# Optimization experiments

Hardware: AMD Instinct MI355X
Metric: run time of the kernel (lower is better)

Reference implementation:

```python
import jax, jax.numpy as jnp
import numpy as np

N = 50000        # nodes
E = 800000       # edges
IN_DIM, HID, OUT = 512, 256, 128
EPS = 1e-5       # PyG LayerNorm eps (added to std)


def setup_inputs() -> dict:
    key = jax.random.key(0)
    ks = jax.random.split(key, 24)
    def lin(k, i, o, scale=0.05):
        kw, kb = jax.random.split(k)
        return (jax.random.normal(kw, (i, o), jnp.float32) * scale,
                jax.random.normal(kb, (o,), jnp.float32) * scale)
    x = jax.random.normal(ks[0], (N, IN_DIM), jnp.float32)
    edge_index = jax.random.randint(ks[1], (2, E), 0, N, jnp.int64)
    Wq1, bq1 = lin(ks[2], IN_DIM, HID)
    Wk1, bk1 = lin(ks[3], IN_DIM, HID)
    Wv1, bv1 = lin(ks[4], IN_DIM, HID)
    Ws1, bs1 = lin(ks[5], IN_DIM, HID)
    g1 = jnp.ones((HID,), jnp.float32)
    be1 = jnp.zeros((HID,), jnp.float32)
    Wq2, bq2 = lin(ks[6], HID, OUT)
    Wk2, bk2 = lin(ks[7], HID, OUT)
    Wv2, bv2 = lin(ks[8], HID, OUT)
    Ws2, bs2 = lin(ks[9], HID, OUT)
    g2 = jnp.ones((OUT,), jnp.float32)
    be2 = jnp.zeros((OUT,), jnp.float32)
    return dict(x=x, Wq1=Wq1, bq1=bq1, Wk1=Wk1, bk1=bk1, Wv1=Wv1, bv1=bv1,
                Ws1=Ws1, bs1=bs1, g1=g1, be1=be1,
                Wq2=Wq2, bq2=bq2, Wk2=Wk2, bk2=bk2, Wv2=Wv2, bv2=bv2,
                Ws2=Ws2, bs2=bs2, g2=g2, be2=be2, edge_index=edge_index)


def transformer_conv(x, edge_index, Wq, bq, Wk, bk, Wv, bv, Ws, bs):
    # PyG TransformerConv, heads=1, concat=True, root_weight=True
    src, dst = edge_index[0], edge_index[1]
    n = x.shape[0]
    d = Wq.shape[1]
    q = x @ Wq + bq                               # [N, d]
    k = x @ Wk + bk
    v = x @ Wv + bv
    score = (q[dst] * k[src]).sum(-1) / jnp.sqrt(jnp.asarray(d, x.dtype))  # [E]
    m = jax.ops.segment_max(score, dst, num_segments=n)     # per-target max
    e = jnp.exp(score - m[dst])
    denom = jax.ops.segment_sum(e, dst, num_segments=n)
    alpha = e / denom[dst]                         # scatter-softmax over in-edges
    agg = jax.ops.segment_sum(alpha[:, None] * v[src], dst, num_segments=n)
    return agg + (x @ Ws + bs)                     # root/skip connection


def graph_layer_norm(h, w, b):
    # PyG LayerNorm mode='graph', no batch: normalize over ALL entries
    h = h - h.mean()
    return h / (h.std() + EPS) * w + b


def reference(x, Wq1, bq1, Wk1, bk1, Wv1, bv1, Ws1, bs1, g1, be1,
              Wq2, bq2, Wk2, bk2, Wv2, bv2, Ws2, bs2, g2, be2, edge_index):
    a1 = graph_layer_norm(
        transformer_conv(x, edge_index, Wq1, bq1, Wk1, bk1, Wv1, bv1, Ws1, bs1),
        g1, be1)
    h1 = jax.nn.elu(a1)  # ELU(alpha=1.0)
    h2 = graph_layer_norm(
        transformer_conv(h1, edge_index, Wq2, bq2, Wk2, bk2, Wv2, bv2, Ws2, bs2),
        g2, be2)
    return h2
```

## Files before the change

kernel.cpp:

```cpp
#include <hip/hip_runtime.h>
#include <stdint.h>
#include <math.h>

#define IN_DIM 512
#define HID    256
#define OUTD   128
#define LN_EPS 1e-5f

typedef unsigned short u16;
typedef unsigned int   u32;
typedef short short8 __attribute__((ext_vector_type(8)));
typedef float f32x4  __attribute__((ext_vector_type(4)));

__device__ __forceinline__ float bf2f(u32 h) {
  union { u32 u; float f; } c; c.u = h << 16; return c.f;
}
__device__ __forceinline__ u16 f2bf(float f) {
  union { float f; u32 u; } c; c.f = f;
  u32 u = c.u;
  return (u16)((u + 0x7FFFu + ((u >> 16) & 1u)) >> 16);
}

__device__ __forceinline__ void gload_lds16(const void* g, void* l) {
  __builtin_amdgcn_global_load_lds((const __attribute__((address_space(1))) void*)g,
                                   (__attribute__((address_space(3))) void*)l, 16, 0, 0);
}

__global__ void k_cvt_f32_bf16_v4(const float* __restrict__ in, u16* __restrict__ out, int n4) {
  int i = blockIdx.x * blockDim.x + threadIdx.x;
  if (i >= n4) return;
  const float4 v = ((const float4*)in)[i];
  ushort4 o;
  o.x = f2bf(v.x); o.y = f2bf(v.y); o.z = f2bf(v.z); o.w = f2bf(v.w);
  ((ushort4*)out)[i] = o;
}

__global__ void k_transpose_w(const float* __restrict__ in, u16* __restrict__ out, int K, int Nw) {
  int idx = blockIdx.x * blockDim.x + threadIdx.x;
  if (idx >= K * Nw) return;
  int n = idx / K, k = idx - n * K;
  out[idx] = f2bf(in[(size_t)k * Nw + n]);
}

__global__ void k_concat4(const float* __restrict__ b0, const float* __restrict__ b1,
                          const float* __restrict__ b2, const float* __restrict__ b3,
                          float* __restrict__ out, int H) {
  int i = blockIdx.x * blockDim.x + threadIdx.x;
  if (i >= 4 * H) return;
  const float* s = (i < H) ? b0 : (i < 2 * H) ? b1 : (i < 3 * H) ? b2 : b3;
  out[i] = s[i & (H - 1)];
}

__global__ void k_hist(const int* __restrict__ dst, int* __restrict__ deg, int E) {
  int e = blockIdx.x * blockDim.x + threadIdx.x;
  if (e < E) atomicAdd(&deg[dst[e]], 1);
}

__global__ void k_block_sum(const int* __restrict__ deg, int* __restrict__ bsum, int n) {
  __shared__ int sm[256];
  int i = blockIdx.x * 256 + threadIdx.x;
  sm[threadIdx.x] = (i < n) ? deg[i] : 0;
  __syncthreads();
  for (int off = 128; off > 0; off >>= 1) {
    if (threadIdx.x < off) sm[threadIdx.x] += sm[threadIdx.x + off];
    __syncthreads();
  }
  if (threadIdx.x == 0) bsum[blockIdx.x] = sm[0];
}

__global__ void k_scan_bsum(const int* __restrict__ bsum, int* __restrict__ boff, int nb) {
  __shared__ int sm[256];
  int t = threadIdx.x;
  int v = (t < nb) ? bsum[t] : 0;
  sm[t] = v;
  __syncthreads();
  for (int off = 1; off < 256; off <<= 1) {
    int tmp = (t >= off) ? sm[t - off] : 0;
    __syncthreads();
    sm[t] += tmp;
    __syncthreads();
  }
  if (t < nb) boff[t] = sm[t] - v;
}

__global__ void k_scan_final(const int* __restrict__ deg, const int* __restrict__ boff,
                             int* __restrict__ offsets, int n, int total) {
  __shared__ int sm[256];
  int t = threadIdx.x;
  int i = blockIdx.x * 256 + t;
  int v = (i < n) ? deg[i] : 0;
  sm[t] = v;
  __syncthreads();
  for (int off = 1; off < 256; off <<= 1) {
    int tmp = (t >= off) ? sm[t - off] : 0;
    __syncthreads();
    sm[t] += tmp;
    __syncthreads();
  }
  if (i < n) offsets[i] = boff[blockIdx.x] + sm[t] - v;
  if (i == 0) offsets[n] = total;
}

__global__ void k_copy_int(const int* __restrict__ in, int* __restrict__ out, int n) {
  int i = blockIdx.x * blockDim.x + threadIdx.x;
  if (i < n) out[i] = in[i];
}

__global__ void k_scatter(const int* __restrict__ src, const int* __restrict__ dst,
                          int* __restrict__ cursor, int* __restrict__ ssrc, int E) {
  int e = blockIdx.x * blockDim.x + threadIdx.x;
  if (e >= E) return;
  int d = dst[e];
  int pos = atomicAdd(&cursor[d], 1);
  ssrc[pos] = src[e];
}

__global__ __launch_bounds__(256) void k_gemm_bf16_nt(
    const u16* __restrict__ A, const u16* __restrict__ Bt, const float* __restrict__ bias,
    u16* __restrict__ C, int M, int K, int Nt) {
  __shared__ __align__(16) u16 As[128 * 32];
  __shared__ __align__(16) u16 Bs[128 * 32];
  const int tid = threadIdx.x;
  const int bm0 = blockIdx.x * 128;
  const int bn0 = blockIdx.y * 128;
  const int wave = tid >> 6, lane = tid & 63;
  const int q = lane >> 4, r16 = lane & 15;
  const int wm = (wave >> 1) * 64, wn = (wave & 1) * 64;

  f32x4 acc[4][4];
#pragma unroll
  for (int i = 0; i < 4; i++)
#pragma unroll
    for (int j = 0; j < 4; j++) acc[i][j] = (f32x4){0.f, 0.f, 0.f, 0.f};

  const int r0 = tid >> 2;
  const int c0 = (tid & 3) * 8;

  for (int kt = 0; kt < K; kt += 32) {
#pragma unroll
    for (int h = 0; h < 2; ++h) {
      int row = r0 + h * 64;
      gload_lds16(A + (size_t)(bm0 + row) * K + kt + c0, &As[row * 32 + c0]);
      gload_lds16(Bt + (size_t)(bn0 + row) * K + kt + c0, &Bs[row * 32 + c0]);
    }
    __syncthreads();
    short8 af[4], bfr[4];
#pragma unroll
    for (int i = 0; i < 4; i++) af[i] = *(const short8*)(&As[(wm + i * 16 + r16) * 32 + q * 8]);
#pragma unroll
    for (int j = 0; j < 4; j++) bfr[j] = *(const short8*)(&Bs[(wn + j * 16 + r16) * 32 + q * 8]);
#pragma unroll
    for (int i = 0; i < 4; i++)
#pragma unroll
      for (int j = 0; j < 4; j++)
        acc[i][j] = __builtin_amdgcn_mfma_f32_16x16x32_bf16(af[i], bfr[j], acc[i][j], 0, 0, 0);
    __syncthreads();
  }

#pragma unroll
  for (int i = 0; i < 4; i++) {
#pragma unroll
    for (int r = 0; r < 4; r++) {
      int grow = bm0 + wm + i * 16 + q * 4 + r;
      if (grow >= M) continue;
      size_t rbase = (size_t)grow * Nt;
#pragma unroll
      for (int j = 0; j < 4; j++) {
        int gcol = bn0 + wn + j * 16 + r16;
        float v = acc[i][j][r] + bias[gcol];
        C[rbase + gcol] = f2bf(v);
      }
    }
  }
}

template <int VPL>
__device__ __forceinline__ void load_bf(const u16* __restrict__ p, int lane, float* f) {
  if constexpr (VPL == 4) {
    uint2 r = *(const uint2*)(p + lane * 4);
    f[0] = bf2f(r.x & 0xffffu); f[1] = bf2f(r.x >> 16);
    f[2] = bf2f(r.y & 0xffffu); f[3] = bf2f(r.y >> 16);
  } else {
    u32 r = *(const u32*)(p + lane * 2);
    f[0] = bf2f(r & 0xffffu); f[1] = bf2f(r >> 16);
  }
}

template <int H, bool OUT_BF16>
__global__ __launch_bounds__(256) void k_conv(
    const u16* __restrict__ qkvs, const int* __restrict__ offsets,
    const int* __restrict__ ssrc, u16* __restrict__ out_bf,
    float* __restrict__ out_f, int n, float scale) {
  constexpr int VPL = H / 64;
  int gw = (blockIdx.x * blockDim.x + threadIdx.x) >> 6;
  int lane = threadIdx.x & 63;
  if (gw >= n) return;
  const u16* base = qkvs + (size_t)gw * (4 * H);
  float qf[VPL];
  load_bf<VPL>(base, lane, qf);
  int beg = offsets[gw], end = offsets[gw + 1];
  float m = -INFINITY, l = 0.f;
  float agg[VPL];
#pragma unroll
  for (int w = 0; w < VPL; w++) agg[w] = 0.f;

  int i = beg;
  for (; i + 4 <= end; i += 4) {
    int s0 = ssrc[i], s1 = ssrc[i + 1], s2 = ssrc[i + 2], s3 = ssrc[i + 3];
    const u16* k0p = qkvs + (size_t)s0 * (4 * H) + H;
    const u16* k1p = qkvs + (size_t)s1 * (4 * H) + H;
    const u16* k2p = qkvs + (size_t)s2 * (4 * H) + H;
    const u16* k3p = qkvs + (size_t)s3 * (4 * H) + H;
    float k0[VPL], k1[VPL], k2[VPL], k3[VPL];
    float v0[VPL], v1[VPL], v2[VPL], v3[VPL];
    load_bf<VPL>(k0p, lane, k0);
    load_bf<VPL>(k1p, lane, k1);
    load_bf<VPL>(k2p, lane, k2);
    load_bf<VPL>(k3p, lane, k3);
    load_bf<VPL>(k0p + H, lane, v0);
    load_bf<VPL>(k1p + H, lane, v1);
    load_bf<VPL>(k2p + H, lane, v2);
    load_bf<VPL>(k3p + H, lane, v3);
    float d0 = 0.f, d1 = 0.f, d2 = 0.f, d3 = 0.f;
#pragma unroll
    for (int w = 0; w < VPL; w++) {
      d0 += qf[w] * k0[w]; d1 += qf[w] * k1[w];
      d2 += qf[w] * k2[w]; d3 += qf[w] * k3[w];
    }
#pragma unroll
    for (int off = 32; off > 0; off >>= 1) {
      d0 += __shfl_xor(d0, off, 64);
      d1 += __shfl_xor(d1, off, 64);
      d2 += __shfl_xor(d2, off, 64);
      d3 += __shfl_xor(d3, off, 64);
    }
    d0 *= scale; d1 *= scale; d2 *= scale; d3 *= scale;
    float cm = fmaxf(fmaxf(d0, d1), fmaxf(d2, d3));
    float nm = fmaxf(m, cm);
    float sc = __expf(m - nm);
    float p0 = __expf(d0 - nm), p1 = __expf(d1 - nm);
    float p2 = __expf(d2 - nm), p3 = __expf(d3 - nm);
    m = nm;
    l = l * sc + (p0 + p1) + (p2 + p3);
#pragma unroll
    for (int w = 0; w < VPL; w++)
      agg[w] = agg[w] * sc + p0 * v0[w] + p1 * v1[w] + p2 * v2[w] + p3 * v3[w];
  }
  for (; i < end; ++i) {
    int s = ssrc[i];
    const u16* kb = qkvs + (size_t)s * (4 * H) + H;
    float kf[VPL], vf[VPL];
    load_bf<VPL>(kb, lane, kf);
    load_bf<VPL>(kb + H, lane, vf);
    float d = 0.f;
#pragma unroll
    for (int w = 0; w < VPL; w++) d += qf[w] * kf[w];
#pragma unroll
    for (int off = 32; off > 0; off >>= 1) d += __shfl_xor(d, off, 64);
    float score = d * scale;
    float nm = fmaxf(m, score);
    float sc = __expf(m - nm);
    float p = __expf(score - nm);
    m = nm;
    l = l * sc + p;
#pragma unroll
    for (int w = 0; w < VPL; w++) agg[w] = agg[w] * sc + p * vf[w];
  }

  float sf[VPL];
  load_bf<VPL>(base + 3 * H, lane, sf);
  float inv = (end > beg) ? 1.f / l : 0.f;
#pragma unroll
  for (int w = 0; w < VPL; w++) {
    float r = agg[w] * inv + sf[w];
    if (OUT_BF16) out_bf[(size_t)gw * H + lane * VPL + w] = f2bf(r);
    else out_f[(size_t)gw * H + lane * VPL + w] = r;
  }
}

__global__ void k_stats_bf16(const u16* __restrict__ a, int n, double* __restrict__ st) {
  float s = 0.f, s2 = 0.f;
  for (int i = blockIdx.x * blockDim.x + threadIdx.x; i < n; i += gridDim.x * blockDim.x) {
    float v = bf2f(a[i]);
    s += v; s2 += v * v;
  }
  __shared__ float sm[256], sm2[256];
  sm[threadIdx.x] = s; sm2[threadIdx.x] = s2;
  __syncthreads();
  for (int off = 128; off > 0; off >>= 1) {
    if (threadIdx.x < off) { sm[threadIdx.x] += sm[threadIdx.x + off]; sm2[threadIdx.x] += sm2[threadIdx.x + off]; }
    __syncthreads();
  }
  if (threadIdx.x == 0) { atomicAdd(&st[0], (double)sm[0]); atomicAdd(&st[1], (double)sm2[0]); }
}

__global__ void k_stats_f32(const float* __restrict__ a, int n, double* __restrict__ st) {
  float s = 0.f, s2 = 0.f;
  for (int i = blockIdx.x * blockDim.x + threadIdx.x; i < n; i += gridDim.x * blockDim.x) {
    float v = a[i];
    s += v; s2 += v * v;
  }
  __shared__ float sm[256], sm2[256];
  sm[threadIdx.x] = s; sm2[threadIdx.x] = s2;
  __syncthreads();
  for (int off = 128; off > 0; off >>= 1) {
    if (threadIdx.x < off) { sm[threadIdx.x] += sm[threadIdx.x + off]; sm2[threadIdx.x] += sm2[threadIdx.x + off]; }
    __syncthreads();
  }
  if (threadIdx.x == 0) { atomicAdd(&st[0], (double)sm[0]); atomicAdd(&st[1], (double)sm2[0]); }
}

__global__ void k_finstats(const double* __restrict__ st, float* __restrict__ fs, double cnt) {
  double mu = st[0] / cnt;
  double var = st[1] / cnt - mu * mu;
  if (var < 0.0) var = 0.0;
  fs[0] = (float)mu;
  fs[1] = (float)(1.0 / (sqrt(var) + (double)LN_EPS));
}

__global__ void k_norm_elu_bf16(const u16* __restrict__ a, const float* __restrict__ g,
                                const float* __restrict__ b, const float* __restrict__ fs,
                                u16* __restrict__ out, int n, int Hmask) {
  int i = blockIdx.x * blockDim.x + threadIdx.x;
  if (i >= n) return;
  int c = i & Hmask;
  float y = (bf2f(a[i]) - fs[0]) * fs[1] * g[c] + b[c];
  y = (y > 0.f) ? y : (__expf(y) - 1.f);
  out[i] = f2bf(y);
}

__global__ void k_norm_f32(float* __restrict__ a, const float* __restrict__ g,
                           const float* __restrict__ b, const float* __restrict__ fs,
                           int n, int Hmask) {
  int i = blockIdx.x * blockDim.x + threadIdx.x;
  if (i >= n) return;
  int c = i & Hmask;
  a[i] = (a[i] - fs[0]) * fs[1] * g[c] + b[c];
}

extern "C" void kernel_launch(void* const* d_in, const int* in_sizes, int n_in,
                              void* d_out, int out_size, void* d_ws, size_t ws_size,
                              hipStream_t stream) {
  const float* x   = (const float*)d_in[0];
  const float* Wq1 = (const float*)d_in[1];  const float* bq1 = (const float*)d_in[2];
  const float* Wk1 = (const float*)d_in[3];  const float* bk1 = (const float*)d_in[4];
  const float* Wv1 = (const float*)d_in[5];  const float* bv1 = (const float*)d_in[6];
  const float* Ws1 = (const float*)d_in[7];  const float* bs1 = (const float*)d_in[8];
  const float* g1  = (const float*)d_in[9];  const float* be1 = (const float*)d_in[10];
  const float* Wq2 = (const float*)d_in[11]; const float* bq2 = (const float*)d_in[12];
  const float* Wk2 = (const float*)d_in[13]; const float* bk2 = (const float*)d_in[14];
  const float* Wv2 = (const float*)d_in[15]; const float* bv2 = (const float*)d_in[16];
  const float* Ws2 = (const float*)d_in[17]; const float* bs2 = (const float*)d_in[18];
  const float* g2  = (const float*)d_in[19]; const float* be2 = (const float*)d_in[20];
  const int*   ei  = (const int*)d_in[21];

  const int N = in_sizes[0] / IN_DIM;
  const int E = in_sizes[21] / 2;
  const int* esrc = ei;
  const int* edst = ei + E;

  char* w = (char*)d_ws;
  auto carve = [&](size_t bytes) { char* p = w; w += (bytes + 255) & ~(size_t)255; return p; };
  u16* x_bf  = (u16*)carve((size_t)N * IN_DIM * 2);
  u16* Wt1   = (u16*)carve((size_t)4 * HID * IN_DIM * 2);
  u16* Wt2   = (u16*)carve((size_t)4 * OUTD * HID * 2);
  float* bc1 = (float*)carve(4 * HID * 4);
  float* bc2 = (float*)carve(4 * OUTD * 4);
  u16* qkvs1 = (u16*)carve((size_t)N * 4 * HID * 2);
  u16* a1    = (u16*)carve((size_t)N * HID * 2);
  int* deg   = (int*)carve((size_t)(N + 1) * 4);
  int* offs  = (int*)carve((size_t)(N + 1) * 4);
  int* cur   = (int*)carve((size_t)(N + 1) * 4);
  int* ssrc  = (int*)carve((size_t)E * 4);
  int* bsum  = (int*)carve(1024);
  int* boff  = (int*)carve(1024);
  double* st = (double*)carve(64);
  float* fs  = (float*)carve(64);
  u16* h1    = x_bf;
  u16* qkvs2 = qkvs1;

  hipMemsetAsync(deg, 0, (size_t)N * 4, stream);
  hipMemsetAsync(st, 0, 64, stream);

  int n4 = N * IN_DIM / 4;
  k_cvt_f32_bf16_v4<<<(n4 + 255) / 256, 256, 0, stream>>>(x, x_bf, n4);
  k_transpose_w<<<(IN_DIM * HID + 255) / 256, 256, 0, stream>>>(Wq1, Wt1 + 0 * (size_t)HID * IN_DIM, IN_DIM, HID);
  k_transpose_w<<<(IN_DIM * HID + 255) / 256, 256, 0, stream>>>(Wk1, Wt1 + 1 * (size_t)HID * IN_DIM, IN_DIM, HID);
  k_transpose_w<<<(IN_DIM * HID + 255) / 256, 256, 0, stream>>>(Wv1, Wt1 + 2 * (size_t)HID * IN_DIM, IN_DIM, HID);
  k_transpose_w<<<(IN_DIM * HID + 255) / 256, 256, 0, stream>>>(Ws1, Wt1 + 3 * (size_t)HID * IN_DIM, IN_DIM, HID);
  k_concat4<<<(4 * HID + 255) / 256, 256, 0, stream>>>(bq1, bk1, bv1, bs1, bc1, HID);
  k_transpose_w<<<(HID * OUTD + 255) / 256, 256, 0, stream>>>(Wq2, Wt2 + 0 * (size_t)OUTD * HID, HID, OUTD);
  k_transpose_w<<<(HID * OUTD + 255) / 256, 256, 0, stream>>>(Wk2, Wt2 + 1 * (size_t)OUTD * HID, HID, OUTD);
  k_transpose_w<<<(HID * OUTD + 255) / 256, 256, 0, stream>>>(Wv2, Wt2 + 2 * (size_t)OUTD * HID, HID, OUTD);
  k_transpose_w<<<(HID * OUTD + 255) / 256, 256, 0, stream>>>(Ws2, Wt2 + 3 * (size_t)OUTD * HID, HID, OUTD);
  k_concat4<<<(4 * OUTD + 255) / 256, 256, 0, stream>>>(bq2, bk2, bv2, bs2, bc2, OUTD);

  int nb = (N + 255) / 256;
  k_hist<<<(E + 255) / 256, 256, 0, stream>>>(edst, deg, E);
  k_block_sum<<<nb, 256, 0, stream>>>(deg, bsum, N);
  k_scan_bsum<<<1, 256, 0, stream>>>(bsum, boff, nb);
  k_scan_final<<<nb, 256, 0, stream>>>(deg, boff, offs, N, E);
  k_copy_int<<<nb, 256, 0, stream>>>(offs, cur, N);
  k_scatter<<<(E + 255) / 256, 256, 0, stream>>>(esrc, edst, cur, ssrc, E);

  dim3 gg1((N + 127) / 128, (4 * HID) / 128);
  k_gemm_bf16_nt<<<gg1, 256, 0, stream>>>(x_bf, Wt1, bc1, qkvs1, N, IN_DIM, 4 * HID);
  k_conv<HID, true><<<(N + 3) / 4, 256, 0, stream>>>(qkvs1, offs, ssrc, a1, nullptr, N,
                                                     1.0f / sqrtf((float)HID));
  k_stats_bf16<<<2048, 256, 0, stream>>>(a1, N * HID, st);
  k_finstats<<<1, 1, 0, stream>>>(st, fs, (double)N * HID);
  k_norm_elu_bf16<<<(N * HID + 255) / 256, 256, 0, stream>>>(a1, g1, be1, fs, h1, N * HID, HID - 1);

  dim3 gg2((N + 127) / 128, (4 * OUTD) / 128);
  k_gemm_bf16_nt<<<gg2, 256, 0, stream>>>(h1, Wt2, bc2, qkvs2, N, HID, 4 * OUTD);
  k_conv<OUTD, false><<<(N + 3) / 4, 256, 0, stream>>>(qkvs2, offs, ssrc, nullptr, (float*)d_out, N,
                                                       1.0f / sqrtf((float)OUTD));
  k_stats_f32<<<2048, 256, 0, stream>>>((const float*)d_out, N * OUTD, st + 2);
  k_finstats<<<1, 1, 0, stream>>>(st + 2, fs + 2, (double)N * OUTD);
  k_norm_f32<<<(N * OUTD + 255) / 256, 256, 0, stream>>>((float*)d_out, g2, be2, fs + 2, N * OUTD, OUTD - 1);
}
```

Before: 772.2 us.

## Fuse prep kernels, split edges across sub-waves in conv, fold stats into conv

Merges the input conversion, weight transposes and bias concatenation into one prep kernel, and the cursor copy into the scan. Restructures the attention conv so each wave handles several edges at once, with sub-groups of lanes loading 16-byte K/V slices, followed by a cross-subgroup online-softmax merge. The layer-norm sum and sum-of-squares are now accumulated inside the conv, which removes the separate stats pass. The normalize kernels are vectorized. The aim is fewer launches, fewer memory passes and better gather memory-level parallelism, at the cost of extra shuffle merges and more complex tail handling.

```diff
diff --git a/kernel.cpp b/kernel.cpp
--- a/kernel.cpp
+++ b/kernel.cpp
@@ -26,29 +26,54 @@
                                    (__attribute__((address_space(3))) void*)l, 16, 0, 0);
 }
 
-__global__ void k_cvt_f32_bf16_v4(const float* __restrict__ in, u16* __restrict__ out, int n4) {
-  int i = blockIdx.x * blockDim.x + threadIdx.x;
-  if (i >= n4) return;
-  const float4 v = ((const float4*)in)[i];
-  ushort4 o;
-  o.x = f2bf(v.x); o.y = f2bf(v.y); o.z = f2bf(v.z); o.w = f2bf(v.w);
-  ((ushort4*)out)[i] = o;
-}
-
-__global__ void k_transpose_w(const float* __restrict__ in, u16* __restrict__ out, int K, int Nw) {
-  int idx = blockIdx.x * blockDim.x + threadIdx.x;
-  if (idx >= K * Nw) return;
-  int n = idx / K, k = idx - n * K;
-  out[idx] = f2bf(in[(size_t)k * Nw + n]);
-}
-
-__global__ void k_concat4(const float* __restrict__ b0, const float* __restrict__ b1,
-                          const float* __restrict__ b2, const float* __restrict__ b3,
-                          float* __restrict__ out, int H) {
-  int i = blockIdx.x * blockDim.x + threadIdx.x;
-  if (i >= 4 * H) return;
-  const float* s = (i < H) ? b0 : (i < 2 * H) ? b1 : (i < 3 * H) ? b2 : b3;
-  out[i] = s[i & (H - 1)];
+__global__ void k_prep(const float* __restrict__ x, u16* __restrict__ x_bf, int n4,
+                       const float* __restrict__ Wq1, const float* __restrict__ Wk1,
+                       const float* __restrict__ Wv1, const float* __restrict__ Ws1,
+                       const float* __restrict__ Wq2, const float* __restrict__ Wk2,
+                       const float* __restrict__ Wv2, const float* __restrict__ Ws2,
+                       u16* __restrict__ Wt1, u16* __restrict__ Wt2,
+                       const float* __restrict__ bq1, const float* __restrict__ bk1,
+                       const float* __restrict__ bv1, const float* __restrict__ bs1,
+                       const float* __restrict__ bq2, const float* __restrict__ bk2,
+                       const float* __restrict__ bv2, const float* __restrict__ bs2,
+                       float* __restrict__ bc1, float* __restrict__ bc2) {
+  const int W1SZ = 4 * HID * IN_DIM;
+  const int W2SZ = 4 * OUTD * HID;
+  int id = blockIdx.x * blockDim.x + threadIdx.x;
+  if (id < n4) {
+    const float4 v = ((const float4*)x)[id];
+    ushort4 o;
+    o.x = f2bf(v.x); o.y = f2bf(v.y); o.z = f2bf(v.z); o.w = f2bf(v.w);
+    ((ushort4*)x_bf)[id] = o;
+    return;
+  }
+  id -= n4;
+  if (id < W1SZ) {
+    int mat = id >> 17, r = id & 131071;
+    int n = r >> 9, k = r & 511;
+    const float* src = (mat == 0) ? Wq1 : (mat == 1) ? Wk1 : (mat == 2) ? Wv1 : Ws1;
+    Wt1[id] = f2bf(src[k * HID + n]);
+    return;
+  }
+  id -= W1SZ;
+  if (id < W2SZ) {
+    int mat = id >> 15, r = id & 32767;
+    int n = r >> 8, k = r & 255;
+    const float* src = (mat == 0) ? Wq2 : (mat == 1) ? Wk2 : (mat == 2) ? Wv2 : Ws2;
+    Wt2[id] = f2bf(src[k * OUTD + n]);
+    return;
+  }
+  id -= W2SZ;
+  if (id < 4 * HID) {
+    const float* s = (id < HID) ? bq1 : (id < 2 * HID) ? bk1 : (id < 3 * HID) ? bv1 : bs1;
+    bc1[id] = s[id & (HID - 1)];
+    return;
+  }
+  id -= 4 * HID;
+  if (id < 4 * OUTD) {
+    const float* s = (id < OUTD) ? bq2 : (id < 2 * OUTD) ? bk2 : (id < 3 * OUTD) ? bv2 : bs2;
+    bc2[id] = s[id & (OUTD - 1)];
+  }
 }
 
 __global__ void k_hist(const int* __restrict__ dst, int* __restrict__ deg, int E) {
@@ -84,7 +109,8 @@
 }
 
 __global__ void k_scan_final(const int* __restrict__ deg, const int* __restrict__ boff,
-                             int* __restrict__ offsets, int n, int total) {
+                             int* __restrict__ offsets, int* __restrict__ cur,
+                             int n, int total) {
   __shared__ int sm[256];
   int t = threadIdx.x;
   int i = blockIdx.x * 256 + t;
@@ -97,13 +123,12 @@
     sm[t] += tmp;
     __syncthreads();
   }
-  if (i < n) offsets[i] = boff[blockIdx.x] + sm[t] - v;
+  if (i < n) {
+    int o = boff[blockIdx.x] + sm[t] - v;
+    offsets[i] = o;
+    cur[i] = o;
+  }
   if (i == 0) offsets[n] = total;
-}
-
-__global__ void k_copy_int(const int* __restrict__ in, int* __restrict__ out, int n) {
-  int i = blockIdx.x * blockDim.x + threadIdx.x;
-  if (i < n) out[i] = in[i];
 }
 
 __global__ void k_scatter(const int* __restrict__ src, const int* __restrict__ dst,
@@ -174,140 +199,193 @@
   }
 }
 
-template <int VPL>
-__device__ __forceinline__ void load_bf(const u16* __restrict__ p, int lane, float* f) {
-  if constexpr (VPL == 4) {
-    uint2 r = *(const uint2*)(p + lane * 4);
-    f[0] = bf2f(r.x & 0xffffu); f[1] = bf2f(r.x >> 16);
-    f[2] = bf2f(r.y & 0xffffu); f[3] = bf2f(r.y >> 16);
-  } else {
-    u32 r = *(const u32*)(p + lane * 2);
-    f[0] = bf2f(r & 0xffffu); f[1] = bf2f(r >> 16);
-  }
-}
-
 template <int H, bool OUT_BF16>
 __global__ __launch_bounds__(256) void k_conv(
     const u16* __restrict__ qkvs, const int* __restrict__ offsets,
     const int* __restrict__ ssrc, u16* __restrict__ out_bf,
-    float* __restrict__ out_f, int n, float scale) {
-  constexpr int VPL = H / 64;
-  int gw = (blockIdx.x * blockDim.x + threadIdx.x) >> 6;
-  int lane = threadIdx.x & 63;
-  if (gw >= n) return;
-  const u16* base = qkvs + (size_t)gw * (4 * H);
-  float qf[VPL];
-  load_bf<VPL>(base, lane, qf);
-  int beg = offsets[gw], end = offsets[gw + 1];
+    float* __restrict__ out_f, int n, float scale, double* __restrict__ st) {
+  constexpr int SUBW = H / 8;
+  constexpr int EPW = 64 / SUBW;
+  constexpr int U = (H == 256) ? 4 : 2;
+
+  const int wave = threadIdx.x >> 6;
+  const int lane = threadIdx.x & 63;
+  const int sub = lane & (SUBW - 1);
+  const int subid = lane >> ((H == 256) ? 5 : 4);
+  const int gw = blockIdx.x * 4 + wave;
+
   float m = -INFINITY, l = 0.f;
-  float agg[VPL];
-#pragma unroll
-  for (int w = 0; w < VPL; w++) agg[w] = 0.f;
-
-  int i = beg;
-  for (; i + 4 <= end; i += 4) {
-    int s0 = ssrc[i], s1 = ssrc[i + 1], s2 = ssrc[i + 2], s3 = ssrc[i + 3];
-    const u16* k0p = qkvs + (size_t)s0 * (4 * H) + H;
-    const u16* k1p = qkvs + (size_t)s1 * (4 * H) + H;
-    const u16* k2p = qkvs + (size_t)s2 * (4 * H) + H;
-    const u16* k3p = qkvs + (size_t)s3 * (4 * H) + H;
-    float k0[VPL], k1[VPL], k2[VPL], k3[VPL];
-    float v0[VPL], v1[VPL], v2[VPL], v3[VPL];
-    load_bf<VPL>(k0p, lane, k0);
-    load_bf<VPL>(k1p, lane, k1);
-    load_bf<VPL>(k2p, lane, k2);
-    load_bf<VPL>(k3p, lane, k3);
-    load_bf<VPL>(k0p + H, lane, v0);
-    load_bf<VPL>(k1p + H, lane, v1);
-    load_bf<VPL>(k2p + H, lane, v2);
-    load_bf<VPL>(k3p + H, lane, v3);
-    float d0 = 0.f, d1 = 0.f, d2 = 0.f, d3 = 0.f;
-#pragma unroll
-    for (int w = 0; w < VPL; w++) {
-      d0 += qf[w] * k0[w]; d1 += qf[w] * k1[w];
-      d2 += qf[w] * k2[w]; d3 += qf[w] * k3[w];
-    }
-#pragma unroll
-    for (int off = 32; off > 0; off >>= 1) {
-      d0 += __shfl_xor(d0, off, 64);
-      d1 += __shfl_xor(d1, off, 64);
-      d2 += __shfl_xor(d2, off, 64);
-      d3 += __shfl_xor(d3, off, 64);
-    }
-    d0 *= scale; d1 *= scale; d2 *= scale; d3 *= scale;
-    float cm = fmaxf(fmaxf(d0, d1), fmaxf(d2, d3));
-    float nm = fmaxf(m, cm);
-    float sc = __expf(m - nm);
-    float p0 = __expf(d0 - nm), p1 = __expf(d1 - nm);
-    float p2 = __expf(d2 - nm), p3 = __expf(d3 - nm);
-    m = nm;
-    l = l * sc + (p0 + p1) + (p2 + p3);
-#pragma unroll
-    for (int w = 0; w < VPL; w++)
-      agg[w] = agg[w] * sc + p0 * v0[w] + p1 * v1[w] + p2 * v2[w] + p3 * v3[w];
-  }
-  for (; i < end; ++i) {
-    int s = ssrc[i];
-    const u16* kb = qkvs + (size_t)s * (4 * H) + H;
-    float kf[VPL], vf[VPL];
-    load_bf<VPL>(kb, lane, kf);
-    load_bf<VPL>(kb + H, lane, vf);
-    float d = 0.f;
-#pragma unroll
-    for (int w = 0; w < VPL; w++) d += qf[w] * kf[w];
-#pragma unroll
-    for (int off = 32; off > 0; off >>= 1) d += __shfl_xor(d, off, 64);
-    float score = d * scale;
-    float nm = fmaxf(m, score);
-    float sc = __expf(m - nm);
-    float p = __expf(score - nm);
-    m = nm;
-    l = l * sc + p;
-#pragma unroll
-    for (int w = 0; w < VPL; w++) agg[w] = agg[w] * sc + p * vf[w];
-  }
-
-  float sf[VPL];
-  load_bf<VPL>(base + 3 * H, lane, sf);
-  float inv = (end > beg) ? 1.f / l : 0.f;
-#pragma unroll
-  for (int w = 0; w < VPL; w++) {
-    float r = agg[w] * inv + sf[w];
-    if (OUT_BF16) out_bf[(size_t)gw * H + lane * VPL + w] = f2bf(r);
-    else out_f[(size_t)gw * H + lane * VPL + w] = r;
-  }
-}
-
-__global__ void k_stats_bf16(const u16* __restrict__ a, int n, double* __restrict__ st) {
+  float agg[8];
+#pragma unroll
+  for (int w = 0; w < 8; w++) agg[w] = 0.f;
+  float r[8];
+#pragma unroll
+  for (int w = 0; w < 8; w++) r[w] = 0.f;
+  bool live = gw < n;
+  int beg = 0, end = 0;
+
+  if (live) {
+    const u16* base = qkvs + (size_t)gw * (4 * H);
+    float qf[8];
+    {
+      uint4 qv = *(const uint4*)(base + sub * 8);
+      const u32 qa[4] = {qv.x, qv.y, qv.z, qv.w};
+#pragma unroll
+      for (int w = 0; w < 4; w++) {
+        qf[2 * w] = bf2f(qa[w] & 0xffffu);
+        qf[2 * w + 1] = bf2f(qa[w] >> 16);
+      }
+    }
+    beg = offsets[gw]; end = offsets[gw + 1];
+
+    int i = beg;
+    for (; i + EPW * U <= end; i += EPW * U) {
+      uint4 kq[U], vq[U];
+      const u16* kp[U];
+#pragma unroll
+      for (int u = 0; u < U; u++) {
+        int s = ssrc[i + u * EPW + subid];
+        kp[u] = qkvs + (size_t)s * (4 * H) + H;
+      }
+#pragma unroll
+      for (int u = 0; u < U; u++) kq[u] = *(const uint4*)(kp[u] + sub * 8);
+#pragma unroll
+      for (int u = 0; u < U; u++) vq[u] = *(const uint4*)(kp[u] + H + sub * 8);
+      float d[U];
+#pragma unroll
+      for (int u = 0; u < U; u++) {
+        const u32 ka[4] = {kq[u].x, kq[u].y, kq[u].z, kq[u].w};
+        float dd = 0.f;
+#pragma unroll
+        for (int w = 0; w < 4; w++) {
+          dd += qf[2 * w] * bf2f(ka[w] & 0xffffu);
+          dd += qf[2 * w + 1] * bf2f(ka[w] >> 16);
+        }
+        d[u] = dd;
+      }
+#pragma unroll
+      for (int off = SUBW / 2; off > 0; off >>= 1)
+#pragma unroll
+        for (int u = 0; u < U; u++) d[u] += __shfl_xor(d[u], off, 64);
+      float cm = -INFINITY;
+#pragma unroll
+      for (int u = 0; u < U; u++) { d[u] *= scale; cm = fmaxf(cm, d[u]); }
+      float nm = fmaxf(m, cm);
+      float sc = __expf(m - nm);
+      float p[U];
+      float ps = 0.f;
+#pragma unroll
+      for (int u = 0; u < U; u++) { p[u] = __expf(d[u] - nm); ps += p[u]; }
+      m = nm;
+      l = l * sc + ps;
+#pragma unroll
+      for (int w = 0; w < 8; w++) {
+        float a = agg[w] * sc;
+#pragma unroll
+        for (int u = 0; u < U; u++) {
+          const u32 vv = ((const u32*)&vq[u])[w >> 1];
+          float vf = bf2f((w & 1) ? (vv >> 16) : (vv & 0xffffu));
+          a += p[u] * vf;
+        }
+        agg[w] = a;
+      }
+    }
+    for (; i < end; i += EPW) {
+      int e = i + subid;
+      bool act = e < end;
+      int s = act ? ssrc[e] : ssrc[i];
+      const u16* kp = qkvs + (size_t)s * (4 * H) + H;
+      uint4 kq = *(const uint4*)(kp + sub * 8);
+      uint4 vq = *(const uint4*)(kp + H + sub * 8);
+      const u32 ka[4] = {kq.x, kq.y, kq.z, kq.w};
+      float d = 0.f;
+#pragma unroll
+      for (int w = 0; w < 4; w++) {
+        d += qf[2 * w] * bf2f(ka[w] & 0xffffu);
+        d += qf[2 * w + 1] * bf2f(ka[w] >> 16);
+      }
+#pragma unroll
+      for (int off = SUBW / 2; off > 0; off >>= 1) d += __shfl_xor(d, off, 64);
+      d = act ? d * scale : -INFINITY;
+      float nm = fmaxf(m, d);
+      bool dead = (nm == -INFINITY);
+      float sc = dead ? 1.f : __expf(m - nm);
+      float p = dead ? 0.f : __expf(d - nm);
+      m = nm;
+      l = l * sc + p;
+#pragma unroll
+      for (int w = 0; w < 8; w++) {
+        const u32 vv = ((const u32*)&vq)[w >> 1];
+        float vf = bf2f((w & 1) ? (vv >> 16) : (vv & 0xffffu));
+        agg[w] = agg[w] * sc + p * vf;
+      }
+    }
+
+#pragma unroll
+    for (int off = SUBW; off < 64; off <<= 1) {
+      float mo = __shfl_xor(m, off, 64);
+      float lo = __shfl_xor(l, off, 64);
+      float M = fmaxf(m, mo);
+      float sa = (M == -INFINITY) ? 0.f : __expf(m - M);
+      float sb = (M == -INFINITY) ? 0.f : __expf(mo - M);
+      l = l * sa + lo * sb;
+#pragma unroll
+      for (int w = 0; w < 8; w++) {
+        float ao = __shfl_xor(agg[w], off, 64);
+        agg[w] = agg[w] * sa + ao * sb;
+      }
+      m = M;
+    }
+
+    float sf[8];
+    {
+      uint4 sv = *(const uint4*)(base + 3 * H + sub * 8);
+      const u32 sa[4] = {sv.x, sv.y, sv.z, sv.w};
+#pragma unroll
+      for (int w = 0; w < 4; w++) {
+        sf[2 * w] = bf2f(sa[w] & 0xffffu);
+        sf[2 * w + 1] = bf2f(sa[w] >> 16);
+      }
+    }
+    float inv = (end > beg) ? 1.f / l : 0.f;
+#pragma unroll
+    for (int w = 0; w < 8; w++) r[w] = agg[w] * inv + sf[w];
+    if (subid == 0) {
+      if (OUT_BF16) {
+        uint4 o;
+        u32* op = (u32*)&o;
+#pragma unroll
+        for (int w = 0; w < 4; w++)
+          op[w] = (u32)f2bf(r[2 * w]) | ((u32)f2bf(r[2 * w + 1]) << 16);
+        *(uint4*)(out_bf + (size_t)gw * H + sub * 8) = o;
+      } else {
+        float4 o0 = {r[0], r[1], r[2], r[3]};
+        float4 o1 = {r[4], r[5], r[6], r[7]};
+        *(float4*)(out_f + (size_t)gw * H + sub * 8) = o0;
+        *(float4*)(out_f + (size_t)gw * H + sub * 8 + 4) = o1;
+      }
+    }
+  }
+
   float s = 0.f, s2 = 0.f;
-  for (int i = blockIdx.x * blockDim.x + threadIdx.x; i < n; i += gridDim.x * blockDim.x) {
-    float v = bf2f(a[i]);
-    s += v; s2 += v * v;
-  }
-  __shared__ float sm[256], sm2[256];
-  sm[threadIdx.x] = s; sm2[threadIdx.x] = s2;
+  if (live && subid == 0) {
+#pragma unroll
+    for (int w = 0; w < 8; w++) { s += r[w]; s2 += r[w] * r[w]; }
+  }
+#pragma unroll
+  for (int off = 32; off > 0; off >>= 1) {
+    s += __shfl_xor(s, off, 64);
+    s2 += __shfl_xor(s2, off, 64);
+  }
+  __shared__ float bs_[8];
+  if (lane == 0) { bs_[wave * 2] = s; bs_[wave * 2 + 1] = s2; }
   __syncthreads();
-  for (int off = 128; off > 0; off >>= 1) {
-    if (threadIdx.x < off) { sm[threadIdx.x] += sm[threadIdx.x + off]; sm2[threadIdx.x] += sm2[threadIdx.x + off]; }
-    __syncthreads();
-  }
-  if (threadIdx.x == 0) { atomicAdd(&st[0], (double)sm[0]); atomicAdd(&st[1], (double)sm2[0]); }
-}
-
-__global__ void k_stats_f32(const float* __restrict__ a, int n, double* __restrict__ st) {
-  float s = 0.f, s2 = 0.f;
-  for (int i = blockIdx.x * blockDim.x + threadIdx.x; i < n; i += gridDim.x * blockDim.x) {
-    float v = a[i];
-    s += v; s2 += v * v;
-  }
-  __shared__ float sm[256], sm2[256];
-  sm[threadIdx.x] = s; sm2[threadIdx.x] = s2;
-  __syncthreads();
-  for (int off = 128; off > 0; off >>= 1) {
-    if (threadIdx.x < off) { sm[threadIdx.x] += sm[threadIdx.x + off]; sm2[threadIdx.x] += sm2[threadIdx.x + off]; }
-    __syncthreads();
-  }
-  if (threadIdx.x == 0) { atomicAdd(&st[0], (double)sm[0]); atomicAdd(&st[1], (double)sm2[0]); }
+  if (wave == 0 && lane == 0) {
+    float ts = bs_[0] + bs_[2] + bs_[4] + bs_[6];
+    float ts2 = bs_[1] + bs_[3] + bs_[5] + bs_[7];
+    atomicAdd(&st[0], (double)ts);
+    atomicAdd(&st[1], (double)ts2);
+  }
 }
 
 __global__ void k_finstats(const double* __restrict__ st, float* __restrict__ fs, double cnt) {
@@ -320,22 +398,42 @@
 
 __global__ void k_norm_elu_bf16(const u16* __restrict__ a, const float* __restrict__ g,
                                 const float* __restrict__ b, const float* __restrict__ fs,
-                                u16* __restrict__ out, int n, int Hmask) {
-  int i = blockIdx.x * blockDim.x + threadIdx.x;
-  if (i >= n) return;
-  int c = i & Hmask;
-  float y = (bf2f(a[i]) - fs[0]) * fs[1] * g[c] + b[c];
-  y = (y > 0.f) ? y : (__expf(y) - 1.f);
-  out[i] = f2bf(y);
+                                u16* __restrict__ out, int n8, int Hmask) {
+  int id = blockIdx.x * blockDim.x + threadIdx.x;
+  if (id >= n8) return;
+  int i8 = id * 8;
+  int cb = i8 & Hmask;
+  uint4 v = *(const uint4*)(a + i8);
+  const u32 va[4] = {v.x, v.y, v.z, v.w};
+  float mu = fs[0], inv = fs[1];
+  uint4 o;
+  u32* op = (u32*)&o;
+#pragma unroll
+  for (int w = 0; w < 4; w++) {
+    float y0 = (bf2f(va[w] & 0xffffu) - mu) * inv * g[cb + 2 * w] + b[cb + 2 * w];
+    float y1 = (bf2f(va[w] >> 16) - mu) * inv * g[cb + 2 * w + 1] + b[cb + 2 * w + 1];
+    y0 = (y0 > 0.f) ? y0 : (__expf(y0) - 1.f);
+    y1 = (y1 > 0.f) ? y1 : (__expf(y1) - 1.f);
+    op[w] = (u32)f2bf(y0) | ((u32)f2bf(y1) << 16);
+  }
+  *(uint4*)(out + i8) = o;
 }
 
 __global__ void k_norm_f32(float* __restrict__ a, const float* __restrict__ g,
                            const float* __restrict__ b, const float* __restrict__ fs,
-                           int n, int Hmask) {
-  int i = blockIdx.x * blockDim.x + threadIdx.x;
-  if (i >= n) return;
-  int c = i & Hmask;
-  a[i] = (a[i] - fs[0]) * fs[1] * g[c] + b[c];
+                           int n4, int Hmask) {
+  int id = blockIdx.x * blockDim.x + threadIdx.x;
+  if (id >= n4) return;
+  int i4 = id * 4;
+  int cb = i4 & Hmask;
+  float4 v = *(const float4*)(a + i4);
+  float mu = fs[0], inv = fs[1];
+  float4 o;
+  o.x = (v.x - mu) * inv * g[cb] + b[cb];
+  o.y = (v.y - mu) * inv * g[cb + 1] + b[cb + 1];
+  o.z = (v.z - mu) * inv * g[cb + 2] + b[cb + 2];
+  o.w = (v.w - mu) * inv * g[cb + 3] + b[cb + 3];
+  *(float4*)(a + i4) = o;
 }
 
 extern "C" void kernel_launch(void* const* d_in, const int* in_sizes, int n_in,
@@ -361,6 +459,8 @@
 
   char* w = (char*)d_ws;
   auto carve = [&](size_t bytes) { char* p = w; w += (bytes + 255) & ~(size_t)255; return p; };
+  int* deg   = (int*)carve((size_t)(N + 1) * 4);
+  double* st = (double*)carve(64);
   u16* x_bf  = (u16*)carve((size_t)N * IN_DIM * 2);
   u16* Wt1   = (u16*)carve((size_t)4 * HID * IN_DIM * 2);
   u16* Wt2   = (u16*)carve((size_t)4 * OUTD * HID * 2);
@@ -368,54 +468,43 @@
   float* bc2 = (float*)carve(4 * OUTD * 4);
   u16* qkvs1 = (u16*)carve((size_t)N * 4 * HID * 2);
   u16* a1    = (u16*)carve((size_t)N * HID * 2);
-  int* deg   = (int*)carve((size_t)(N + 1) * 4);
   int* offs  = (int*)carve((size_t)(N + 1) * 4);
   int* cur   = (int*)carve((size_t)(N + 1) * 4);
   int* ssrc  = (int*)carve((size_t)E * 4);
   int* bsum  = (int*)carve(1024);
   int* boff  = (int*)carve(1024);
-  double* st = (double*)carve(64);
   float* fs  = (float*)carve(64);
   u16* h1    = x_bf;
   u16* qkvs2 = qkvs1;
 
-  hipMemsetAsync(deg, 0, (size_t)N * 4, stream);
-  hipMemsetAsync(st, 0, 64, stream);
+  hipMemsetAsync(deg, 0, (size_t)((char*)st - (char*)deg) + 64, stream);
 
   int n4 = N * IN_DIM / 4;
-  k_cvt_f32_bf16_v4<<<(n4 + 255) / 256, 256, 0, stream>>>(x, x_bf, n4);
-  k_transpose_w<<<(IN_DIM * HID + 255) / 256, 256, 0, stream>>>(Wq1, Wt1 + 0 * (size_t)HID * IN_DIM, IN_DIM, HID);
-  k_transpose_w<<<(IN_DIM * HID + 255) / 256, 256, 0, stream>>>(Wk1, Wt1 + 1 * (size_t)HID * IN_DIM, IN_DIM, HID);
-  k_transpose_w<<<(IN_DIM * HID + 255) / 256, 256, 0, stream>>>(Wv1, Wt1 + 2 * (size_t)HID * IN_DIM, IN_DIM, HID);
-  k_transpose_w<<<(IN_DIM * HID + 255) / 256, 256, 0, stream>>>(Ws1, Wt1 + 3 * (size_t)HID * IN_DIM, IN_DIM, HID);
-  k_concat4<<<(4 * HID + 255) / 256, 256, 0, stream>>>(bq1, bk1, bv1, bs1, bc1, HID);
-  k_transpose_w<<<(HID * OUTD + 255) / 256, 256, 0, stream>>>(Wq2, Wt2 + 0 * (size_t)OUTD * HID, HID, OUTD);
-  k_transpose_w<<<(HID * OUTD + 255) / 256, 256, 0, stream>>>(Wk2, Wt2 + 1 * (size_t)OUTD * HID, HID, OUTD);
-  k_transpose_w<<<(HID * OUTD + 255) / 256, 256, 0, stream>>>(Wv2, Wt2 + 2 * (size_t)OUTD * HID, HID, OUTD);
-  k_transpose_w<<<(HID * OUTD + 255) / 256, 256, 0, stream>>>(Ws2, Wt2 + 3 * (size_t)OUTD * HID, HID, OUTD);
-  k_concat4<<<(4 * OUTD + 255) / 256, 256, 0, stream>>>(bq2, bk2, bv2, bs2, bc2, OUTD);
+  int prep_total = n4 + 4 * HID * IN_DIM + 4 * OUTD * HID + 4 * HID + 4 * OUTD;
+  k_prep<<<(prep_total + 255) / 256, 256, 0, stream>>>(
+      x, x_bf, n4, Wq1, Wk1, Wv1, Ws1, Wq2, Wk2, Wv2, Ws2, Wt1, Wt2,
+      bq1, bk1, bv1, bs1, bq2, bk2, bv2, bs2, bc1, bc2);
 
   int nb = (N + 255) / 256;
   k_hist<<<(E + 255) / 256, 256, 0, stream>>>(edst, deg, E);
   k_block_sum<<<nb, 256, 0, stream>>>(deg, bsum, N);
   k_scan_bsum<<<1, 256, 0, stream>>>(bsum, boff, nb);
-  k_scan_final<<<nb, 256, 0, stream>>>(deg, boff, offs, N, E);
-  k_copy_int<<<nb, 256, 0, stream>>>(offs, cur, N);
+  k_scan_final<<<nb, 256, 0, stream>>>(deg, boff, offs, cur, N, E);
   k_scatter<<<(E + 255) / 256, 256, 0, stream>>>(esrc, edst, cur, ssrc, E);
 
   dim3 gg1((N + 127) / 128, (4 * HID) / 128);
   k_gemm_bf16_nt<<<gg1, 256, 0, stream>>>(x_bf, Wt1, bc1, qkvs1, N, IN_DIM, 4 * HID);
   k_conv<HID, true><<<(N + 3) / 4, 256, 0, stream>>>(qkvs1, offs, ssrc, a1, nullptr, N,
-                                                     1.0f / sqrtf((float)HID));
-  k_stats_bf16<<<2048, 256, 0, stream>>>(a1, N * HID, st);
+                                                     1.0f / sqrtf((float)HID), st);
   k_finstats<<<1, 1, 0, stream>>>(st, fs, (double)N * HID);
-  k_norm_elu_bf16<<<(N * HID + 255) / 256, 256, 0, stream>>>(a1, g1, be1, fs, h1, N * HID, HID - 1);
+  k_norm_elu_bf16<<<(N * HID / 8 + 255) / 256, 256, 0, stream>>>(a1, g1, be1, fs, h1,
+                                                                 N * HID / 8, HID - 1);
 
   dim3 gg2((N + 127) / 128, (4 * OUTD) / 128);
   k_gemm_bf16_nt<<<gg2, 256, 0, stream>>>(h1, Wt2, bc2, qkvs2, N, HID, 4 * OUTD);
-  k_conv<OUTD, false><<<(N + 3) / 4, 256, 0, stream>>>(qkvs2, offs, ssrc, nullptr, (float*)d_out, N,
-                                                       1.0f / sqrtf((float)OUTD));
-  k_stats_f32<<<2048, 256, 0, stream>>>((const float*)d_out, N * OUTD, st + 2);
+  k_conv<OUTD, false><<<(N + 3) / 4, 256, 0, stream>>>(qkvs2, offs, ssrc, nullptr, (float*)d_out,
+                                                       N, 1.0f / sqrtf((float)OUTD), st + 2);
   k_finstats<<<1, 1, 0, stream>>>(st + 2, fs + 2, (double)N * OUTD);
-  k_norm_f32<<<(N * OUTD + 255) / 256, 256, 0, stream>>>((float*)d_out, g2, be2, fs + 2, N * OUTD, OUTD - 1);
-}
+  k_norm_f32<<<(N * OUTD / 4 + 255) / 256, 256, 0, stream>>>((float*)d_out, g2, be2, fs + 2,
+                                                             N * OUTD / 4, OUTD - 1);
+}
```

New measurement: 1.085 ms. 40.5% more time.

## Merge prep launches, tile weight transposes, vectorize stats and norm kernels

Applied to the files above, without the earlier changes.

Merges the input conversion and bias concatenation into a single launch. Replaces eight per-weight transposes with two shared-memory tiled transposes that cover all four weights via blockIdx.z. Folds the cursor copy into the scan and the two memsets into one. Vectorizes the stats and normalization kernels to 16-byte loads and stores. The aim is fewer launches and better memory coalescing on the small elementwise passes, at the cost of assuming sizes divisible by 8 and 4.

```diff
diff --git a/kernel.cpp b/kernel.cpp
--- a/kernel.cpp
+++ b/kernel.cpp
@@ -26,29 +26,49 @@
                                    (__attribute__((address_space(3))) void*)l, 16, 0, 0);
 }
 
-__global__ void k_cvt_f32_bf16_v4(const float* __restrict__ in, u16* __restrict__ out, int n4) {
-  int i = blockIdx.x * blockDim.x + threadIdx.x;
-  if (i >= n4) return;
-  const float4 v = ((const float4*)in)[i];
-  ushort4 o;
-  o.x = f2bf(v.x); o.y = f2bf(v.y); o.z = f2bf(v.z); o.w = f2bf(v.w);
-  ((ushort4*)out)[i] = o;
-}
-
-__global__ void k_transpose_w(const float* __restrict__ in, u16* __restrict__ out, int K, int Nw) {
-  int idx = blockIdx.x * blockDim.x + threadIdx.x;
-  if (idx >= K * Nw) return;
-  int n = idx / K, k = idx - n * K;
-  out[idx] = f2bf(in[(size_t)k * Nw + n]);
-}
-
-__global__ void k_concat4(const float* __restrict__ b0, const float* __restrict__ b1,
-                          const float* __restrict__ b2, const float* __restrict__ b3,
-                          float* __restrict__ out, int H) {
-  int i = blockIdx.x * blockDim.x + threadIdx.x;
-  if (i >= 4 * H) return;
-  const float* s = (i < H) ? b0 : (i < 2 * H) ? b1 : (i < 3 * H) ? b2 : b3;
-  out[i] = s[i & (H - 1)];
+__global__ void k_prep(const float* __restrict__ x, u16* __restrict__ x_bf, int n4,
+                       const float* __restrict__ bq1, const float* __restrict__ bk1,
+                       const float* __restrict__ bv1, const float* __restrict__ bs1,
+                       const float* __restrict__ bq2, const float* __restrict__ bk2,
+                       const float* __restrict__ bv2, const float* __restrict__ bs2,
+                       float* __restrict__ bc1, float* __restrict__ bc2) {
+  int id = blockIdx.x * blockDim.x + threadIdx.x;
+  if (id < n4) {
+    const float4 v = ((const float4*)x)[id];
+    ushort4 o;
+    o.x = f2bf(v.x); o.y = f2bf(v.y); o.z = f2bf(v.z); o.w = f2bf(v.w);
+    ((ushort4*)x_bf)[id] = o;
+    return;
+  }
+  id -= n4;
+  if (id < 4 * HID) {
+    const float* s = (id < HID) ? bq1 : (id < 2 * HID) ? bk1 : (id < 3 * HID) ? bv1 : bs1;
+    bc1[id] = s[id & (HID - 1)];
+    return;
+  }
+  id -= 4 * HID;
+  if (id < 4 * OUTD) {
+    const float* s = (id < OUTD) ? bq2 : (id < 2 * OUTD) ? bk2 : (id < 3 * OUTD) ? bv2 : bs2;
+    bc2[id] = s[id & (OUTD - 1)];
+  }
+}
+
+__global__ void k_transpose4(const float* __restrict__ s0, const float* __restrict__ s1,
+                             const float* __restrict__ s2, const float* __restrict__ s3,
+                             u16* __restrict__ out, int K, int Nw) {
+  __shared__ u16 t[32][33];
+  const float* src = (blockIdx.z == 0) ? s0 : (blockIdx.z == 1) ? s1
+                     : (blockIdx.z == 2) ? s2 : s3;
+  u16* dst = out + (size_t)blockIdx.z * K * Nw;
+  int k0 = blockIdx.x * 32, n0 = blockIdx.y * 32;
+  int tx = threadIdx.x, ty = threadIdx.y;
+#pragma unroll
+  for (int i = 0; i < 32; i += 8)
+    t[ty + i][tx] = f2bf(src[(size_t)(k0 + ty + i) * Nw + n0 + tx]);
+  __syncthreads();
+#pragma unroll
+  for (int i = 0; i < 32; i += 8)
+    dst[(size_t)(n0 + ty + i) * K + k0 + tx] = t[tx][ty + i];
 }
 
 __global__ void k_hist(const int* __restrict__ dst, int* __restrict__ deg, int E) {
@@ -84,7 +104,8 @@
 }
 
 __global__ void k_scan_final(const int* __restrict__ deg, const int* __restrict__ boff,
-                             int* __restrict__ offsets, int n, int total) {
+                             int* __restrict__ offsets, int* __restrict__ cur,
+                             int n, int total) {
   __shared__ int sm[256];
   int t = threadIdx.x;
   int i = blockIdx.x * 256 + t;
@@ -97,13 +118,12 @@
     sm[t] += tmp;
     __syncthreads();
   }
-  if (i < n) offsets[i] = boff[blockIdx.x] + sm[t] - v;
+  if (i < n) {
+    int o = boff[blockIdx.x] + sm[t] - v;
+    offsets[i] = o;
+    cur[i] = o;
+  }
   if (i == 0) offsets[n] = total;
-}
-
-__global__ void k_copy_int(const int* __restrict__ in, int* __restrict__ out, int n) {
-  int i = blockIdx.x * blockDim.x + threadIdx.x;
-  if (i < n) out[i] = in[i];
 }
 
 __global__ void k_scatter(const int* __restrict__ src, const int* __restrict__ dst,
@@ -278,11 +298,16 @@
   }
 }
 
-__global__ void k_stats_bf16(const u16* __restrict__ a, int n, double* __restrict__ st) {
+__global__ void k_stats_bf16(const u16* __restrict__ a, int n8, double* __restrict__ st) {
   float s = 0.f, s2 = 0.f;
-  for (int i = blockIdx.x * blockDim.x + threadIdx.x; i < n; i += gridDim.x * blockDim.x) {
-    float v = bf2f(a[i]);
-    s += v; s2 += v * v;
+  for (int i = blockIdx.x * blockDim.x + threadIdx.x; i < n8; i += gridDim.x * blockDim.x) {
+    uint4 v = ((const uint4*)a)[i];
+    const u32 va[4] = {v.x, v.y, v.z, v.w};
+#pragma unroll
+    for (int w = 0; w < 4; w++) {
+      float x0 = bf2f(va[w] & 0xffffu), x1 = bf2f(va[w] >> 16);
+      s += x0 + x1; s2 += x0 * x0 + x1 * x1;
+    }
   }
   __shared__ float sm[256], sm2[256];
   sm[threadIdx.x] = s; sm2[threadIdx.x] = s2;
@@ -294,11 +319,12 @@
   if (threadIdx.x == 0) { atomicAdd(&st[0], (double)sm[0]); atomicAdd(&st[1], (double)sm2[0]); }
 }
 
-__global__ void k_stats_f32(const float* __restrict__ a, int n, double* __restrict__ st) {
+__global__ void k_stats_f32(const float* __restrict__ a, int n4, double* __restrict__ st) {
   float s = 0.f, s2 = 0.f;
-  for (int i = blockIdx.x * blockDim.x + threadIdx.x; i < n; i += gridDim.x * blockDim.x) {
-    float v = a[i];
-    s += v; s2 += v * v;
+  for (int i = blockIdx.x * blockDim.x + threadIdx.x; i < n4; i += gridDim.x * blockDim.x) {
+    float4 v = ((const float4*)a)[i];
+    s += v.x + v.y + v.z + v.w;
+    s2 += v.x * v.x + v.y * v.y + v.z * v.z + v.w * v.w;
   }
   __shared__ float sm[256], sm2[256];
   sm[threadIdx.x] = s; sm2[threadIdx.x] = s2;
@@ -320,22 +346,42 @@
 
 __global__ void k_norm_elu_bf16(const u16* __restrict__ a, const float* __restrict__ g,
                                 const float* __restrict__ b, const float* __restrict__ fs,
-                                u16* __restrict__ out, int n, int Hmask) {
-  int i = blockIdx.x * blockDim.x + threadIdx.x;
-  if (i >= n) return;
-  int c = i & Hmask;
-  float y = (bf2f(a[i]) - fs[0]) * fs[1] * g[c] + b[c];
-  y = (y > 0.f) ? y : (__expf(y) - 1.f);
-  out[i] = f2bf(y);
+                                u16* __restrict__ out, int n8, int Hmask) {
+  int id = blockIdx.x * blockDim.x + threadIdx.x;
+  if (id >= n8) return;
+  int i8 = id * 8;
+  int cb = i8 & Hmask;
+  uint4 v = *(const uint4*)(a + i8);
+  const u32 va[4] = {v.x, v.y, v.z, v.w};
+  float mu = fs[0], inv = fs[1];
+  uint4 o;
+  u32* op = (u32*)&o;
+#pragma unroll
+  for (int w = 0; w < 4; w++) {
+    float y0 = (bf2f(va[w] & 0xffffu) - mu) * inv * g[cb + 2 * w] + b[cb + 2 * w];
+    float y1 = (bf2f(va[w] >> 16) - mu) * inv * g[cb + 2 * w + 1] + b[cb + 2 * w + 1];
+    y0 = (y0 > 0.f) ? y0 : (__expf(y0) - 1.f);
+    y1 = (y1 > 0.f) ? y1 : (__expf(y1) - 1.f);
+    op[w] = (u32)f2bf(y0) | ((u32)f2bf(y1) << 16);
+  }
+  *(uint4*)(out + i8) = o;
 }
 
 __global__ void k_norm_f32(float* __restrict__ a, const float* __restrict__ g,
                            const float* __restrict__ b, const float* __restrict__ fs,
-                           int n, int Hmask) {
-  int i = blockIdx.x * blockDim.x + threadIdx.x;
-  if (i >= n) return;
-  int c = i & Hmask;
-  a[i] = (a[i] - fs[0]) * fs[1] * g[c] + b[c];
+                           int n4, int Hmask) {
+  int id = blockIdx.x * blockDim.x + threadIdx.x;
+  if (id >= n4) return;
+  int i4 = id * 4;
+  int cb = i4 & Hmask;
+  float4 v = *(const float4*)(a + i4);
+  float mu = fs[0], inv = fs[1];
+  float4 o;
+  o.x = (v.x - mu) * inv * g[cb] + b[cb];
+  o.y = (v.y - mu) * inv * g[cb + 1] + b[cb + 1];
+  o.z = (v.z - mu) * inv * g[cb + 2] + b[cb + 2];
+  o.w = (v.w - mu) * inv * g[cb + 3] + b[cb + 3];
+  *(float4*)(a + i4) = o;
 }
 
 extern "C" void kernel_launch(void* const* d_in, const int* in_sizes, int n_in,
@@ -361,6 +407,8 @@
 
   char* w = (char*)d_ws;
   auto carve = [&](size_t bytes) { char* p = w; w += (bytes + 255) & ~(size_t)255; return p; };
+  int* deg   = (int*)carve((size_t)(N + 1) * 4);
+  double* st = (double*)carve(64);
   u16* x_bf  = (u16*)carve((size_t)N * IN_DIM * 2);
   u16* Wt1   = (u16*)carve((size_t)4 * HID * IN_DIM * 2);
   u16* Wt2   = (u16*)carve((size_t)4 * OUTD * HID * 2);
@@ -368,54 +416,49 @@
   float* bc2 = (float*)carve(4 * OUTD * 4);
   u16* qkvs1 = (u16*)carve((size_t)N * 4 * HID * 2);
   u16* a1    = (u16*)carve((size_t)N * HID * 2);
-  int* deg   = (int*)carve((size_t)(N + 1) * 4);
   int* offs  = (int*)carve((size_t)(N + 1) * 4);
   int* cur   = (int*)carve((size_t)(N + 1) * 4);
   int* ssrc  = (int*)carve((size_t)E * 4);
   int* bsum  = (int*)carve(1024);
   int* boff  = (int*)carve(1024);
-  double* st = (double*)carve(64);
   float* fs  = (float*)carve(64);
   u16* h1    = x_bf;
   u16* qkvs2 = qkvs1;
 
-  hipMemsetAsync(deg, 0, (size_t)N * 4, stream);
-  hipMemsetAsync(st, 0, 64, stream);
+  hipMemsetAsync(deg, 0, (size_t)((char*)st - (char*)deg) + 64, stream);
 
   int n4 = N * IN_DIM / 4;
-  k_cvt_f32_bf16_v4<<<(n4 + 255) / 256, 256, 0, stream>>>(x, x_bf, n4);
-  k_transpose_w<<<(IN_DIM * HID + 255) / 256, 256, 0, stream>>>(Wq1, Wt1 + 0 * (size_t)HID * IN_DIM, IN_DIM, HID);
-  k_transpose_w<<<(IN_DIM * HID + 255) / 256, 256, 0, stream>>>(Wk1, Wt1 + 1 * (size_t)HID * IN_DIM, IN_DIM, HID);
-  k_transpose_w<<<(IN_DIM * HID + 255) / 256, 256, 0, stream>>>(Wv1, Wt1 + 2 * (size_t)HID * IN_DIM, IN_DIM, HID);
-  k_transpose_w<<<(IN_DIM * HID + 255) / 256, 256, 0, stream>>>(Ws1, Wt1 + 3 * (size_t)HID * IN_DIM, IN_DIM, HID);
-  k_concat4<<<(4 * HID + 255) / 256, 256, 0, stream>>>(bq1, bk1, bv1, bs1, bc1, HID);
-  k_transpose_w<<<(HID * OUTD + 255) / 256, 256, 0, stream>>>(Wq2, Wt2 + 0 * (size_t)OUTD * HID, HID, OUTD);
-  k_transpose_w<<<(HID * OUTD + 255) / 256, 256, 0, stream>>>(Wk2, Wt2 + 1 * (size_t)OUTD * HID, HID, OUTD);
-  k_transpose_w<<<(HID * OUTD + 255) / 256, 256, 0, stream>>>(Wv2, Wt2 + 2 * (size_t)OUTD * HID, HID, OUTD);
-  k_transpose_w<<<(HID * OUTD + 255) / 256, 256, 0, stream>>>(Ws2, Wt2 + 3 * (size_t)OUTD * HID, HID, OUTD);
-  k_concat4<<<(4 * OUTD + 255) / 256, 256, 0, stream>>>(bq2, bk2, bv2, bs2, bc2, OUTD);
+  int prep_total = n4 + 4 * HID + 4 * OUTD;
+  k_prep<<<(prep_total + 255) / 256, 256, 0, stream>>>(
+      x, x_bf, n4, bq1, bk1, bv1, bs1, bq2, bk2, bv2, bs2, bc1, bc2);
+  dim3 tb(32, 8);
+  dim3 tg1(IN_DIM / 32, HID / 32, 4);
+  k_transpose4<<<tg1, tb, 0, stream>>>(Wq1, Wk1, Wv1, Ws1, Wt1, IN_DIM, HID);
+  dim3 tg2(HID / 32, OUTD / 32, 4);
+  k_transpose4<<<tg2, tb, 0, stream>>>(Wq2, Wk2, Wv2, Ws2, Wt2, HID, OUTD);
 
   int nb = (N + 255) / 256;
   k_hist<<<(E + 255) / 256, 256, 0, stream>>>(edst, deg, E);
   k_block_sum<<<nb, 256, 0, stream>>>(deg, bsum, N);
   k_scan_bsum<<<1, 256, 0, stream>>>(bsum, boff, nb);
-  k_scan_final<<<nb, 256, 0, stream>>>(deg, boff, offs, N, E);
-  k_copy_int<<<nb, 256, 0, stream>>>(offs, cur, N);
+  k_scan_final<<<nb, 256, 0, stream>>>(deg, boff, offs, cur, N, E);
   k_scatter<<<(E + 255) / 256, 256, 0, stream>>>(esrc, edst, cur, ssrc, E);
 
   dim3 gg1((N + 127) / 128, (4 * HID) / 128);
   k_gemm_bf16_nt<<<gg1, 256, 0, stream>>>(x_bf, Wt1, bc1, qkvs1, N, IN_DIM, 4 * HID);
   k_conv<HID, true><<<(N + 3) / 4, 256, 0, stream>>>(qkvs1, offs, ssrc, a1, nullptr, N,
                                                      1.0f / sqrtf((float)HID));
-  k_stats_bf16<<<2048, 256, 0, stream>>>(a1, N * HID, st);
+  k_stats_bf16<<<2048, 256, 0, stream>>>(a1, N * HID / 8, st);
   k_finstats<<<1, 1, 0, stream>>>(st, fs, (double)N * HID);
-  k_norm_elu_bf16<<<(N * HID + 255) / 256, 256, 0, stream>>>(a1, g1, be1, fs, h1, N * HID, HID - 1);
+  k_norm_elu_bf16<<<(N * HID / 8 + 255) / 256, 256, 0, stream>>>(a1, g1, be1, fs, h1,
+                                                                 N * HID / 8, HID - 1);
 
   dim3 gg2((N + 127) / 128, (4 * OUTD) / 128);
   k_gemm_bf16_nt<<<gg2, 256, 0, stream>>>(h1, Wt2, bc2, qkvs2, N, HID, 4 * OUTD);
-  k_conv<OUTD, false><<<(N + 3) / 4, 256, 0, stream>>>(qkvs2, offs, ssrc, nullptr, (float*)d_out, N,
-                                                       1.0f / sqrtf((float)OUTD));
-  k_stats_f32<<<2048, 256, 0, stream>>>((const float*)d_out, N * OUTD, st + 2);
+  k_conv<OUTD, false><<<(N + 3) / 4, 256, 0, stream>>>(qkvs2, offs, ssrc, nullptr, (float*)d_out,
+                                                       N, 1.0f / sqrtf((float)OUTD));
+  k_stats_f32<<<2048, 256, 0, stream>>>((const float*)d_out, N * OUTD / 4, st + 2);
   k_finstats<<<1, 1, 0, stream>>>(st + 2, fs + 2, (double)N * OUTD);
-  k_norm_f32<<<(N * OUTD + 255) / 256, 256, 0, stream>>>((float*)d_out, g2, be2, fs + 2, N * OUTD, OUTD - 1);
-}
+  k_norm_f32<<<(N * OUTD / 4 + 255) / 256, 256, 0, stream>>>((float*)d_out, g2, be2, fs + 2,
+                                                             N * OUTD / 4, OUTD - 1);
+}
```

Measured after the change: 734.1 us. 1.05x faster.
